# Kernel tuning notes

Measured on AMD Instinct MI355X. Metric: run time of the kernel, lower is better.

The kernel has to match this reference:

```python
import jax, jax.numpy as jnp
from jax import lax
import numpy as np

T = 16  # decode_times
NEG_SLOPE = 0.01  # LeakyReLU default


def setup_inputs() -> dict:
    key = jax.random.key(0)
    ks = jax.random.split(key, 8)
    H = 256  # hidden_size
    C = 256  # input_size
    O = 2    # linear_output_size
    s = 1.0 / np.sqrt(H)
    return {
        "x": jax.random.normal(ks[0], (8, C, 40, 40), jnp.float32),
        "hx": jnp.zeros((12800, H), jnp.float32),
        "cx": jnp.zeros((12800, H), jnp.float32),
        "W_ih": jax.random.uniform(ks[1], (4 * H, C), jnp.float32, -s, s),
        "W_hh": jax.random.uniform(ks[2], (4 * H, H), jnp.float32, -s, s),
        "b_ih": jax.random.uniform(ks[3], (4 * H,), jnp.float32, -s, s),
        "b_hh": jax.random.uniform(ks[4], (4 * H,), jnp.float32, -s, s),
        "W_lin": jax.random.uniform(ks[5], (O, H), jnp.float32, -s, s),
        "b_lin": jax.random.uniform(ks[6], (O,), jnp.float32, -s, s),
    }


def reference(x, hx, cx, W_ih, W_hh, b_ih, b_hh, W_lin, b_lin):
    bs, c, h, w = x.shape
    # BSxCxHxW -> (BS*H*W, C): same flattening as permute(0,2,3,1).reshape(-1, C)
    xf = jnp.transpose(x, (0, 2, 3, 1)).reshape(-1, c)
    # Input projection is identical every step (same x fed each time)
    x_proj = xf @ W_ih.T + b_ih + b_hh  # [N, 4H]

    def step(carry, _):
        hx, cx = carry
        gates = x_proj + hx @ W_hh.T  # [N, 4H]
        i, f, g, o = jnp.split(gates, 4, axis=-1)  # torch LSTMCell gate order
        i = jax.nn.sigmoid(i)
        f = jax.nn.sigmoid(f)
        g = jnp.tanh(g)
        o = jax.nn.sigmoid(o)
        cx = f * cx + i * g
        hx = o * jnp.tanh(cx)
        return (hx, cx), hx

    _, outs = lax.scan(step, (hx, cx), None, length=T)  # [T, N, H]
    # Dropout(0.1) is identity in eval mode; LeakyReLU then Linear head
    y = jax.nn.leaky_relu(outs, NEG_SLOPE)
    y = jnp.einsum('tnh,oh->tno', y, W_lin) + b_lin  # [T, N, O]
    y = y.reshape(T, bs, h, w, -1)
    return jnp.transpose(y, (1, 2, 3, 0, 4))  # [BS, H, W, T, O]
```

## Files before the change

### kernel.cpp

```cpp
#include <hip/hip_runtime.h>
#include <stdint.h>
#include <stddef.h>

typedef _Float16 half_t;
typedef half_t half8  __attribute__((ext_vector_type(8)));
typedef half_t half4v __attribute__((ext_vector_type(4)));
typedef float  f32x4  __attribute__((ext_vector_type(4)));

__device__ __forceinline__ float fast_sigmoid(float x) {
    float e = __builtin_amdgcn_exp2f(-1.44269504f * x);
    return __builtin_amdgcn_rcpf(1.0f + e);
}
__device__ __forceinline__ float fast_tanh(float x) {
    float e = __builtin_amdgcn_exp2f(2.88539008f * x);
    return 1.0f - 2.0f * __builtin_amdgcn_rcpf(1.0f + e);
}

__global__ __launch_bounds__(64) void shuffle_w_kernel(
    const float* __restrict__ W, half_t* __restrict__ out)
{
    const int blk = blockIdx.x;
    const int T = blk >> 3, kt = blk & 7;
    const int l = threadIdx.x;
    const int j = T * 16 + (l & 15);
    const int k0 = kt * 32 + ((l >> 4) << 3);
    half8 v;
#pragma unroll
    for (int e = 0; e < 8; ++e) v[e] = (half_t)W[j * 256 + k0 + e];
    *reinterpret_cast<half8*>(out + (size_t)(blk * 64 + l) * 8) = v;
}

__device__ __forceinline__ void gemm_pass(
    f32x4* acc, const half_t* __restrict__ lhx,
    const half_t* Ws, int Ta, int Tb, int Tc, int Td,
    int lm, int lg, int l)
{
    asm volatile("" : "+v"(Ws));
    const half_t* bp[4] = {
        Ws + (size_t)((Ta * 8) * 64 + l) * 8,
        Ws + (size_t)((Tb * 8) * 64 + l) * 8,
        Ws + (size_t)((Tc * 8) * 64 + l) * 8,
        Ws + (size_t)((Td * 8) * 64 + l) * 8 };
    half8 bA[4], bB[4];
#pragma unroll
    for (int n = 0; n < 4; ++n) bA[n] = *reinterpret_cast<const half8*>(bp[n]);

#pragma unroll 1
    for (int kt2 = 0; kt2 < 4; ++kt2) {
        const int kt = kt2 * 2;
#pragma unroll
        for (int n = 0; n < 4; ++n)
            bB[n] = *reinterpret_cast<const half8*>(bp[n] + (kt + 1) * 512);
        {
            half8 a[4];
#pragma unroll
            for (int mt = 0; mt < 4; ++mt) {
                const int p = mt * 16 + lm;
                const int k = (kt * 32 + lg * 8) ^ ((p & 7) << 4);
                a[mt] = *reinterpret_cast<const half8*>(&lhx[p * 256 + k]);
            }
#pragma unroll
            for (int n = 0; n < 4; ++n)
#pragma unroll
                for (int mt = 0; mt < 4; ++mt)
                    acc[mt * 4 + n] = __builtin_amdgcn_mfma_f32_16x16x32_f16(
                        a[mt], bA[n], acc[mt * 4 + n], 0, 0, 0);
        }
        __builtin_amdgcn_sched_barrier(0);
#pragma unroll
        for (int n = 0; n < 4; ++n)
            bA[n] = *reinterpret_cast<const half8*>(bp[n] + ((kt + 2) & 7) * 512);
        {
            half8 a[4];
#pragma unroll
            for (int mt = 0; mt < 4; ++mt) {
                const int p = mt * 16 + lm;
                const int k = ((kt + 1) * 32 + lg * 8) ^ ((p & 7) << 4);
                a[mt] = *reinterpret_cast<const half8*>(&lhx[p * 256 + k]);
            }
#pragma unroll
            for (int n = 0; n < 4; ++n)
#pragma unroll
                for (int mt = 0; mt < 4; ++mt)
                    acc[mt * 4 + n] = __builtin_amdgcn_mfma_f32_16x16x32_f16(
                        a[mt], bB[n], acc[mt * 4 + n], 0, 0, 0);
        }
        __builtin_amdgcn_sched_barrier(0);
    }
}

__global__ __launch_bounds__(512)
void lstm_kernel(
    const float* __restrict__ x,
    const float* __restrict__ hx0,
    const float* __restrict__ cx0,
    const float* __restrict__ b_ih,
    const float* __restrict__ b_hh,
    const float* __restrict__ W_lin,
    const float* __restrict__ b_lin,
    const half_t* __restrict__ Wih_s,
    const half_t* __restrict__ Whh_s,
    float* __restrict__ out)
{
    __shared__ __align__(16) half_t lds_hx[64 * 256];
    __shared__ __align__(16) half_t lds_xp[8 * 32 * 64 * 4];

    const int tid = threadIdx.x;
    const int w  = tid >> 6;
    const int l  = tid & 63;
    const int lm = l & 15;
    const int lg = l >> 4;
    const int w2 = w * 2;

    const int row0 = blockIdx.x * 64;
    const int bb_  = row0 / 1600;
    const int p0   = row0 % 1600;

    {
        const float* xin = x + (size_t)bb_ * 409600 + p0;
        for (int it = 0; it < 32; ++it) {
            int idx = it * 512 + tid;
            int p = idx & 63, c = idx >> 6;
            lds_hx[p * 256 + (c ^ ((p & 7) << 4))] = (half_t)xin[c * 1600 + p];
        }
    }
    __syncthreads();

    f32x4 acc[16];

#pragma unroll 1
    for (int pass = 0; pass < 2; ++pass) {
        const int gA = pass ? 0 : 16;
        const int gB = pass ? 32 : 48;
        const int Ta = gA + w2, Tb = Ta + 1;
        const int Tc = gB + w2, Td = Tc + 1;
        const int Tt[4] = {Ta, Tb, Tc, Td};
#pragma unroll
        for (int n = 0; n < 4; ++n) {
            int col = Tt[n] * 16 + lm;
            float bias = b_ih[col] + b_hh[col];
#pragma unroll
            for (int mt = 0; mt < 4; ++mt)
                acc[mt * 4 + n] = (f32x4){bias, bias, bias, bias};
        }
        gemm_pass(acc, lds_hx, Wih_s, Ta, Tb, Tc, Td, lm, lg, l);
#pragma unroll
        for (int f = 0; f < 16; ++f) {
            half4v xv;
#pragma unroll
            for (int r = 0; r < 4; ++r) xv[r] = (half_t)acc[f][r];
            *reinterpret_cast<half4v*>(
                &lds_xp[((w * 32 + pass * 16 + f) * 64 + l) * 4]) = xv;
        }
    }
    __syncthreads();

    {
        const float* hin = hx0 + (size_t)row0 * 256;
        for (int it = 0; it < 32; ++it) {
            int idx = it * 512 + tid;
            int c = idx & 255, p = idx >> 8;
            lds_hx[p * 256 + (c ^ ((p & 7) << 4))] = (half_t)hin[p * 256 + c];
        }
    }
    float cxr[32];
#pragma unroll
    for (int mt = 0; mt < 4; ++mt)
#pragma unroll
        for (int j = 0; j < 2; ++j)
#pragma unroll
            for (int r = 0; r < 4; ++r) {
                int p = mt * 16 + lg * 4 + r;
                int c = w * 32 + j * 16 + lm;
                cxr[(mt * 2 + j) * 4 + r] = cx0[(size_t)(row0 + p) * 256 + c];
            }
    const float blin0 = b_lin[0], blin1 = b_lin[1];
    __syncthreads();

#pragma unroll 1
    for (int t = 0; t < 16; ++t) {
        half4v og[8];

#pragma unroll
        for (int fc = 0; fc < 16; fc += 4) {
#pragma unroll
            for (int f = fc; f < fc + 4; ++f) {
                half4v u = *reinterpret_cast<const half4v*>(
                    &lds_xp[((w * 32 + f) * 64 + l) * 4]);
#pragma unroll
                for (int r = 0; r < 4; ++r) acc[f][r] = (float)u[r];
            }
            __builtin_amdgcn_sched_barrier(0);
        }
        gemm_pass(acc, lds_hx, Whh_s, 16 + w2, 17 + w2, 48 + w2, 49 + w2,
                  lm, lg, l);
#pragma unroll
        for (int mt = 0; mt < 4; ++mt)
#pragma unroll
            for (int j = 0; j < 2; ++j)
#pragma unroll
                for (int r = 0; r < 4; ++r) {
                    float fv = acc[mt * 4 + 0 + j][r];
                    float ov = acc[mt * 4 + 2 + j][r];
                    cxr[(mt * 2 + j) * 4 + r] *= fast_sigmoid(fv);
                    og[mt * 2 + j][r] = (half_t)ov;
                }
        __builtin_amdgcn_sched_barrier(0);

#pragma unroll
        for (int fc = 0; fc < 16; fc += 4) {
#pragma unroll
            for (int f = fc; f < fc + 4; ++f) {
                half4v u = *reinterpret_cast<const half4v*>(
                    &lds_xp[((w * 32 + 16 + f) * 64 + l) * 4]);
#pragma unroll
                for (int r = 0; r < 4; ++r) acc[f][r] = (float)u[r];
            }
            __builtin_amdgcn_sched_barrier(0);
        }
        gemm_pass(acc, lds_hx, Whh_s, w2, w2 + 1, 32 + w2, 33 + w2,
                  lm, lg, l);

        __syncthreads();

#pragma unroll
        for (int mt = 0; mt < 4; ++mt)
#pragma unroll
            for (int j = 0; j < 2; ++j)
#pragma unroll
                for (int r = 0; r < 4; ++r) {
                    const int ci = (mt * 2 + j) * 4 + r;
                    float iv = acc[mt * 4 + 0 + j][r];
                    float gv = acc[mt * 4 + 2 + j][r];
                    float cxn = cxr[ci] + fast_sigmoid(iv) * fast_tanh(gv);
                    cxr[ci] = cxn;
                    float so = fast_sigmoid((float)og[mt * 2 + j][r]);
                    float h = so * fast_tanh(cxn);
                    int p  = mt * 16 + lg * 4 + r;
                    int cc = w * 32 + j * 16 + lm;
                    lds_hx[p * 256 + (cc ^ ((p & 7) << 4))] = (half_t)h;
                }
        __syncthreads();

        {
            const int p = tid >> 3;
            const int o = (tid >> 2) & 1;
            const int q = tid & 3;
            const float* wl = W_lin + o * 256 + q * 64;
            asm volatile("" : "+v"(wl));
            float s = 0.0f;
#pragma unroll 2
            for (int cb = 0; cb < 16; ++cb) {
                int c0 = q * 64 + cb * 4;
                half4v u = *reinterpret_cast<const half4v*>(
                    &lds_hx[p * 256 + (c0 ^ ((p & 7) << 4))]);
                float4 wv = *reinterpret_cast<const float4*>(wl + cb * 4);
                float h0 = (float)u[0], h1 = (float)u[1];
                float h2 = (float)u[2], h3 = (float)u[3];
                s += fmaxf(h0, 0.01f * h0) * wv.x;
                s += fmaxf(h1, 0.01f * h1) * wv.y;
                s += fmaxf(h2, 0.01f * h2) * wv.z;
                s += fmaxf(h3, 0.01f * h3) * wv.w;
            }
            s += __shfl_xor(s, 1);
            s += __shfl_xor(s, 2);
            if (q == 0)
                out[((size_t)(row0 + p) * 16 + t) * 2 + o] =
                    s + (o ? blin1 : blin0);
        }
    }
}

extern "C" void kernel_launch(void* const* d_in, const int* in_sizes, int n_in,
                              void* d_out, int out_size, void* d_ws, size_t ws_size,
                              hipStream_t stream)
{
    const float* x    = (const float*)d_in[0];
    const float* hx   = (const float*)d_in[1];
    const float* cx   = (const float*)d_in[2];
    const float* Wih  = (const float*)d_in[3];
    const float* Whh  = (const float*)d_in[4];
    const float* bih  = (const float*)d_in[5];
    const float* bhh  = (const float*)d_in[6];
    const float* Wlin = (const float*)d_in[7];
    const float* blin = (const float*)d_in[8];
    float* out = (float*)d_out;

    half_t* wih_s = (half_t*)d_ws;
    half_t* whh_s = wih_s + 1024 * 256;

    shuffle_w_kernel<<<512, 64, 0, stream>>>(Wih, wih_s);
    shuffle_w_kernel<<<512, 64, 0, stream>>>(Whh, whh_s);
    lstm_kernel<<<200, 512, 0, stream>>>(x, hx, cx, bih, bhh, Wlin, blin,
                                         wih_s, whh_s, out);
}
```

Measured before the change: 253.6 us.

## Interleave output head and gate epilogue with recurrent GEMM MFMA passes

The gemm_pass loop is fully unrolled and takes a per-k-step callback, so non-MFMA work can be interleaved with the matrix instructions. The linear head for step t-1 now runs inside the first recurrent GEMM of step t, and the forget/output gate sigmoids run inside the second GEMM using a separate accumulator set. A final head pass handles the last timestep after the loop. This aims to hide VALU and LDS work behind MFMA latency and drops one barrier-separated phase per step, at the cost of a second accumulator array and higher register pressure, which could spill or lower occupancy.

```diff
diff --git a/kernel.cpp b/kernel.cpp
--- a/kernel.cpp
+++ b/kernel.cpp
@@ -30,10 +30,11 @@
     *reinterpret_cast<half8*>(out + (size_t)(blk * 64 + l) * 8) = v;
 }
 
+template <typename CoWork>
 __device__ __forceinline__ void gemm_pass(
     f32x4* acc, const half_t* __restrict__ lhx,
     const half_t* Ws, int Ta, int Tb, int Tc, int Td,
-    int lm, int lg, int l)
+    int lm, int lg, int l, CoWork&& cowork)
 {
     asm volatile("" : "+v"(Ws));
     const half_t* bp[4] = {
@@ -41,49 +42,34 @@
         Ws + (size_t)((Tb * 8) * 64 + l) * 8,
         Ws + (size_t)((Tc * 8) * 64 + l) * 8,
         Ws + (size_t)((Td * 8) * 64 + l) * 8 };
-    half8 bA[4], bB[4];
-#pragma unroll
-    for (int n = 0; n < 4; ++n) bA[n] = *reinterpret_cast<const half8*>(bp[n]);
-
-#pragma unroll 1
-    for (int kt2 = 0; kt2 < 4; ++kt2) {
-        const int kt = kt2 * 2;
+    half8 bC[4], bN[4];
+#pragma unroll
+    for (int n = 0; n < 4; ++n) bC[n] = *reinterpret_cast<const half8*>(bp[n]);
+
+#pragma unroll
+    for (int kt = 0; kt < 8; ++kt) {
+        if (kt < 7) {
+#pragma unroll
+            for (int n = 0; n < 4; ++n)
+                bN[n] = *reinterpret_cast<const half8*>(bp[n] + (kt + 1) * 512);
+        }
+        half8 a[4];
+#pragma unroll
+        for (int mt = 0; mt < 4; ++mt) {
+            const int p = mt * 16 + lm;
+            const int k = (kt * 32 + lg * 8) ^ ((p & 7) << 4);
+            a[mt] = *reinterpret_cast<const half8*>(&lhx[p * 256 + k]);
+        }
 #pragma unroll
         for (int n = 0; n < 4; ++n)
-            bB[n] = *reinterpret_cast<const half8*>(bp[n] + (kt + 1) * 512);
-        {
-            half8 a[4];
-#pragma unroll
-            for (int mt = 0; mt < 4; ++mt) {
-                const int p = mt * 16 + lm;
-                const int k = (kt * 32 + lg * 8) ^ ((p & 7) << 4);
-                a[mt] = *reinterpret_cast<const half8*>(&lhx[p * 256 + k]);
-            }
-#pragma unroll
-            for (int n = 0; n < 4; ++n)
-#pragma unroll
-                for (int mt = 0; mt < 4; ++mt)
-                    acc[mt * 4 + n] = __builtin_amdgcn_mfma_f32_16x16x32_f16(
-                        a[mt], bA[n], acc[mt * 4 + n], 0, 0, 0);
-        }
-        __builtin_amdgcn_sched_barrier(0);
-#pragma unroll
-        for (int n = 0; n < 4; ++n)
-            bA[n] = *reinterpret_cast<const half8*>(bp[n] + ((kt + 2) & 7) * 512);
-        {
-            half8 a[4];
-#pragma unroll
-            for (int mt = 0; mt < 4; ++mt) {
-                const int p = mt * 16 + lm;
-                const int k = ((kt + 1) * 32 + lg * 8) ^ ((p & 7) << 4);
-                a[mt] = *reinterpret_cast<const half8*>(&lhx[p * 256 + k]);
-            }
-#pragma unroll
-            for (int n = 0; n < 4; ++n)
-#pragma unroll
-                for (int mt = 0; mt < 4; ++mt)
-                    acc[mt * 4 + n] = __builtin_amdgcn_mfma_f32_16x16x32_f16(
-                        a[mt], bB[n], acc[mt * 4 + n], 0, 0, 0);
+#pragma unroll
+            for (int mt = 0; mt < 4; ++mt)
+                acc[mt * 4 + n] = __builtin_amdgcn_mfma_f32_16x16x32_f16(
+                    a[mt], bC[n], acc[mt * 4 + n], 0, 0, 0);
+        cowork(kt);
+        if (kt < 7) {
+#pragma unroll
+            for (int n = 0; n < 4; ++n) bC[n] = bN[n];
         }
         __builtin_amdgcn_sched_barrier(0);
     }
@@ -126,7 +112,8 @@
     }
     __syncthreads();
 
-    f32x4 acc[16];
+    f32x4 accA[16], accB[16];
+    auto nocw = [](int) {};
 
 #pragma unroll 1
     for (int pass = 0; pass < 2; ++pass) {
@@ -141,14 +128,14 @@
             float bias = b_ih[col] + b_hh[col];
 #pragma unroll
             for (int mt = 0; mt < 4; ++mt)
-                acc[mt * 4 + n] = (f32x4){bias, bias, bias, bias};
-        }
-        gemm_pass(acc, lds_hx, Wih_s, Ta, Tb, Tc, Td, lm, lg, l);
+                accA[mt * 4 + n] = (f32x4){bias, bias, bias, bias};
+        }
+        gemm_pass(accA, lds_hx, Wih_s, Ta, Tb, Tc, Td, lm, lg, l, nocw);
 #pragma unroll
         for (int f = 0; f < 16; ++f) {
             half4v xv;
 #pragma unroll
-            for (int r = 0; r < 4; ++r) xv[r] = (half_t)acc[f][r];
+            for (int r = 0; r < 4; ++r) xv[r] = (half_t)accA[f][r];
             *reinterpret_cast<half4v*>(
                 &lds_xp[((w * 32 + pass * 16 + f) * 64 + l) * 4]) = xv;
         }
@@ -175,12 +162,47 @@
                 cxr[(mt * 2 + j) * 4 + r] = cx0[(size_t)(row0 + p) * 256 + c];
             }
     const float blin0 = b_lin[0], blin1 = b_lin[1];
+    const int ph = tid >> 3;
+    const int ho = (tid >> 2) & 1;
+    const int hq = tid & 3;
     __syncthreads();
 
 #pragma unroll 1
     for (int t = 0; t < 16; ++t) {
         half4v og[8];
 
+        const float* wl = W_lin + ho * 256 + hq * 64;
+        asm volatile("" : "+v"(wl));
+        float hs = 0.0f;
+        float4 hwv0, hwv1;
+        if (t > 0) {
+            hwv0 = *reinterpret_cast<const float4*>(wl + 0);
+            hwv1 = *reinterpret_cast<const float4*>(wl + 4);
+        }
+        auto head_cw = [&](int wi) {
+            if (t > 0) {
+#pragma unroll
+                for (int ii = 0; ii < 2; ++ii) {
+                    int cb = wi * 2 + ii;
+                    int c0 = hq * 64 + cb * 4;
+                    half4v u = *reinterpret_cast<const half4v*>(
+                        &lds_hx[ph * 256 + (c0 ^ ((ph & 7) << 4))]);
+                    float4 wv = ii ? hwv1 : hwv0;
+                    if (cb + 2 < 16) {
+                        float4 nx = *reinterpret_cast<const float4*>(
+                            wl + (cb + 2) * 4);
+                        if (ii) hwv1 = nx; else hwv0 = nx;
+                    }
+                    float h0 = (float)u[0], h1 = (float)u[1];
+                    float h2 = (float)u[2], h3 = (float)u[3];
+                    hs += fmaxf(h0, 0.01f * h0) * wv.x;
+                    hs += fmaxf(h1, 0.01f * h1) * wv.y;
+                    hs += fmaxf(h2, 0.01f * h2) * wv.z;
+                    hs += fmaxf(h3, 0.01f * h3) * wv.w;
+                }
+            }
+        };
+
 #pragma unroll
         for (int fc = 0; fc < 16; fc += 4) {
 #pragma unroll
@@ -188,24 +210,31 @@
                 half4v u = *reinterpret_cast<const half4v*>(
                     &lds_xp[((w * 32 + f) * 64 + l) * 4]);
 #pragma unroll
-                for (int r = 0; r < 4; ++r) acc[f][r] = (float)u[r];
+                for (int r = 0; r < 4; ++r) accA[f][r] = (float)u[r];
             }
             __builtin_amdgcn_sched_barrier(0);
         }
-        gemm_pass(acc, lds_hx, Whh_s, 16 + w2, 17 + w2, 48 + w2, 49 + w2,
-                  lm, lg, l);
-#pragma unroll
-        for (int mt = 0; mt < 4; ++mt)
-#pragma unroll
-            for (int j = 0; j < 2; ++j)
-#pragma unroll
-                for (int r = 0; r < 4; ++r) {
-                    float fv = acc[mt * 4 + 0 + j][r];
-                    float ov = acc[mt * 4 + 2 + j][r];
-                    cxr[(mt * 2 + j) * 4 + r] *= fast_sigmoid(fv);
-                    og[mt * 2 + j][r] = (half_t)ov;
-                }
-        __builtin_amdgcn_sched_barrier(0);
+        gemm_pass(accA, lds_hx, Whh_s, 16 + w2, 17 + w2, 48 + w2, 49 + w2,
+                  lm, lg, l, head_cw);
+        if (t > 0) {
+            hs += __shfl_xor(hs, 1);
+            hs += __shfl_xor(hs, 2);
+            if (hq == 0)
+                out[((size_t)(row0 + ph) * 16 + (t - 1)) * 2 + ho] =
+                    hs + (ho ? blin1 : blin0);
+        }
+
+        auto epiA_cw = [&](int wi) {
+#pragma unroll
+            for (int k = 0; k < 4; ++k) {
+                int v = wi * 4 + k;
+                int mt = v >> 3, j = (v >> 2) & 1, r = v & 3;
+                float fv = accA[mt * 4 + 0 + j][r];
+                float ov = accA[mt * 4 + 2 + j][r];
+                cxr[(mt * 2 + j) * 4 + r] *= fast_sigmoid(fv);
+                og[mt * 2 + j][r] = (half_t)fast_sigmoid(ov);
+            }
+        };
 
 #pragma unroll
         for (int fc = 0; fc < 16; fc += 4) {
@@ -214,12 +243,12 @@
                 half4v u = *reinterpret_cast<const half4v*>(
                     &lds_xp[((w * 32 + 16 + f) * 64 + l) * 4]);
 #pragma unroll
-                for (int r = 0; r < 4; ++r) acc[f][r] = (float)u[r];
+                for (int r = 0; r < 4; ++r) accB[f][r] = (float)u[r];
             }
             __builtin_amdgcn_sched_barrier(0);
         }
-        gemm_pass(acc, lds_hx, Whh_s, w2, w2 + 1, 32 + w2, 33 + w2,
-                  lm, lg, l);
+        gemm_pass(accB, lds_hx, Whh_s, w2, w2 + 1, 32 + w2, 33 + w2,
+                  lm, lg, l, epiA_cw);
 
         __syncthreads();
 
@@ -230,44 +259,40 @@
 #pragma unroll
                 for (int r = 0; r < 4; ++r) {
                     const int ci = (mt * 2 + j) * 4 + r;
-                    float iv = acc[mt * 4 + 0 + j][r];
-                    float gv = acc[mt * 4 + 2 + j][r];
+                    float iv = accB[mt * 4 + 0 + j][r];
+                    float gv = accB[mt * 4 + 2 + j][r];
                     float cxn = cxr[ci] + fast_sigmoid(iv) * fast_tanh(gv);
                     cxr[ci] = cxn;
-                    float so = fast_sigmoid((float)og[mt * 2 + j][r]);
-                    float h = so * fast_tanh(cxn);
+                    float h = (float)og[mt * 2 + j][r] * fast_tanh(cxn);
                     int p  = mt * 16 + lg * 4 + r;
                     int cc = w * 32 + j * 16 + lm;
                     lds_hx[p * 256 + (cc ^ ((p & 7) << 4))] = (half_t)h;
                 }
         __syncthreads();
-
-        {
-            const int p = tid >> 3;
-            const int o = (tid >> 2) & 1;
-            const int q = tid & 3;
-            const float* wl = W_lin + o * 256 + q * 64;
-            asm volatile("" : "+v"(wl));
-            float s = 0.0f;
+    }
+
+    {
+        const float* wl = W_lin + ho * 256 + hq * 64;
+        asm volatile("" : "+v"(wl));
+        float s = 0.0f;
 #pragma unroll 2
-            for (int cb = 0; cb < 16; ++cb) {
-                int c0 = q * 64 + cb * 4;
-                half4v u = *reinterpret_cast<const half4v*>(
-                    &lds_hx[p * 256 + (c0 ^ ((p & 7) << 4))]);
-                float4 wv = *reinterpret_cast<const float4*>(wl + cb * 4);
-                float h0 = (float)u[0], h1 = (float)u[1];
-                float h2 = (float)u[2], h3 = (float)u[3];
-                s += fmaxf(h0, 0.01f * h0) * wv.x;
-                s += fmaxf(h1, 0.01f * h1) * wv.y;
-                s += fmaxf(h2, 0.01f * h2) * wv.z;
-                s += fmaxf(h3, 0.01f * h3) * wv.w;
-            }
-            s += __shfl_xor(s, 1);
-            s += __shfl_xor(s, 2);
-            if (q == 0)
-                out[((size_t)(row0 + p) * 16 + t) * 2 + o] =
-                    s + (o ? blin1 : blin0);
-        }
+        for (int cb = 0; cb < 16; ++cb) {
+            int c0 = hq * 64 + cb * 4;
+            half4v u = *reinterpret_cast<const half4v*>(
+                &lds_hx[ph * 256 + (c0 ^ ((ph & 7) << 4))]);
+            float4 wv = *reinterpret_cast<const float4*>(wl + cb * 4);
+            float h0 = (float)u[0], h1 = (float)u[1];
+            float h2 = (float)u[2], h3 = (float)u[3];
+            s += fmaxf(h0, 0.01f * h0) * wv.x;
+            s += fmaxf(h1, 0.01f * h1) * wv.y;
+            s += fmaxf(h2, 0.01f * h2) * wv.z;
+            s += fmaxf(h3, 0.01f * h3) * wv.w;
+        }
+        s += __shfl_xor(s, 1);
+        s += __shfl_xor(s, 2);
+        if (hq == 0)
+            out[((size_t)(row0 + ph) * 16 + 15) * 2 + ho] =
+                s + (ho ? blin1 : blin0);
     }
 }
 
```

Measured after the change: 318.2 us. 25.5% more time.

## Overlap linear head of previous step with first recurrent GEMM pass

Applied to the files above, without the earlier changes.

The LeakyReLU+Linear head for step t-1 now runs interleaved with the MFMA loop of the first W_hh GEMM pass at step t, through a per-k-tile callback. It no longer runs as a separate phase after the hidden-state update barrier, and the last step's head runs after the loop. The aim is to hide the head's LDS reads, W_lin loads and FMAs under matrix-core work and remove one serialized phase per step. The cost is higher register pressure from the prefetched weights and accumulator inside the GEMM loop, which could reduce scheduling quality.

```diff
diff --git a/kernel.cpp b/kernel.cpp
--- a/kernel.cpp
+++ b/kernel.cpp
@@ -30,10 +30,11 @@
     *reinterpret_cast<half8*>(out + (size_t)(blk * 64 + l) * 8) = v;
 }
 
+template <typename CoWork>
 __device__ __forceinline__ void gemm_pass(
     f32x4* acc, const half_t* __restrict__ lhx,
     const half_t* Ws, int Ta, int Tb, int Tc, int Td,
-    int lm, int lg, int l)
+    int lm, int lg, int l, CoWork&& cowork)
 {
     asm volatile("" : "+v"(Ws));
     const half_t* bp[4] = {
@@ -66,6 +67,7 @@
                     acc[mt * 4 + n] = __builtin_amdgcn_mfma_f32_16x16x32_f16(
                         a[mt], bA[n], acc[mt * 4 + n], 0, 0, 0);
         }
+        cowork(kt);
         __builtin_amdgcn_sched_barrier(0);
 #pragma unroll
         for (int n = 0; n < 4; ++n)
@@ -85,6 +87,7 @@
                     acc[mt * 4 + n] = __builtin_amdgcn_mfma_f32_16x16x32_f16(
                         a[mt], bB[n], acc[mt * 4 + n], 0, 0, 0);
         }
+        cowork(kt + 1);
         __builtin_amdgcn_sched_barrier(0);
     }
 }
@@ -127,6 +130,7 @@
     __syncthreads();
 
     f32x4 acc[16];
+    auto nocw = [](int) {};
 
 #pragma unroll 1
     for (int pass = 0; pass < 2; ++pass) {
@@ -143,7 +147,7 @@
             for (int mt = 0; mt < 4; ++mt)
                 acc[mt * 4 + n] = (f32x4){bias, bias, bias, bias};
         }
-        gemm_pass(acc, lds_hx, Wih_s, Ta, Tb, Tc, Td, lm, lg, l);
+        gemm_pass(acc, lds_hx, Wih_s, Ta, Tb, Tc, Td, lm, lg, l, nocw);
 #pragma unroll
         for (int f = 0; f < 16; ++f) {
             half4v xv;
@@ -175,12 +179,47 @@
                 cxr[(mt * 2 + j) * 4 + r] = cx0[(size_t)(row0 + p) * 256 + c];
             }
     const float blin0 = b_lin[0], blin1 = b_lin[1];
+    const int ph = tid >> 3;
+    const int ho = (tid >> 2) & 1;
+    const int hq = tid & 3;
     __syncthreads();
 
 #pragma unroll 1
     for (int t = 0; t < 16; ++t) {
         half4v og[8];
 
+        const float* wl = W_lin + ho * 256 + hq * 64;
+        asm volatile("" : "+v"(wl));
+        float hs = 0.0f;
+        float4 hwv0, hwv1;
+        if (t > 0) {
+            hwv0 = *reinterpret_cast<const float4*>(wl + 0);
+            hwv1 = *reinterpret_cast<const float4*>(wl + 4);
+        }
+        auto head_cw = [&](int wi) {
+            if (t > 0) {
+#pragma unroll
+                for (int ii = 0; ii < 2; ++ii) {
+                    int cb = wi * 2 + ii;
+                    int c0 = hq * 64 + cb * 4;
+                    half4v u = *reinterpret_cast<const half4v*>(
+                        &lds_hx[ph * 256 + (c0 ^ ((ph & 7) << 4))]);
+                    float4 wv = ii ? hwv1 : hwv0;
+                    if (cb + 2 < 16) {
+                        float4 nx = *reinterpret_cast<const float4*>(
+                            wl + (cb + 2) * 4);
+                        if (ii) hwv1 = nx; else hwv0 = nx;
+                    }
+                    float h0 = (float)u[0], h1 = (float)u[1];
+                    float h2 = (float)u[2], h3 = (float)u[3];
+                    hs += fmaxf(h0, 0.01f * h0) * wv.x;
+                    hs += fmaxf(h1, 0.01f * h1) * wv.y;
+                    hs += fmaxf(h2, 0.01f * h2) * wv.z;
+                    hs += fmaxf(h3, 0.01f * h3) * wv.w;
+                }
+            }
+        };
+
 #pragma unroll
         for (int fc = 0; fc < 16; fc += 4) {
 #pragma unroll
@@ -193,7 +232,15 @@
             __builtin_amdgcn_sched_barrier(0);
         }
         gemm_pass(acc, lds_hx, Whh_s, 16 + w2, 17 + w2, 48 + w2, 49 + w2,
-                  lm, lg, l);
+                  lm, lg, l, head_cw);
+        if (t > 0) {
+            hs += __shfl_xor(hs, 1);
+            hs += __shfl_xor(hs, 2);
+            if (hq == 0)
+                out[((size_t)(row0 + ph) * 16 + (t - 1)) * 2 + ho] =
+                    hs + (ho ? blin1 : blin0);
+        }
+
 #pragma unroll
         for (int mt = 0; mt < 4; ++mt)
 #pragma unroll
@@ -219,7 +266,7 @@
             __builtin_amdgcn_sched_barrier(0);
         }
         gemm_pass(acc, lds_hx, Whh_s, w2, w2 + 1, 32 + w2, 33 + w2,
-                  lm, lg, l);
+                  lm, lg, l, nocw);
 
         __syncthreads();
 
@@ -241,33 +288,30 @@
                     lds_hx[p * 256 + (cc ^ ((p & 7) << 4))] = (half_t)h;
                 }
         __syncthreads();
-
-        {
-            const int p = tid >> 3;
-            const int o = (tid >> 2) & 1;
-            const int q = tid & 3;
-            const float* wl = W_lin + o * 256 + q * 64;
-            asm volatile("" : "+v"(wl));
-            float s = 0.0f;
+    }
+
+    {
+        const float* wl = W_lin + ho * 256 + hq * 64;
+        asm volatile("" : "+v"(wl));
+        float s = 0.0f;
 #pragma unroll 2
-            for (int cb = 0; cb < 16; ++cb) {
-                int c0 = q * 64 + cb * 4;
-                half4v u = *reinterpret_cast<const half4v*>(
-                    &lds_hx[p * 256 + (c0 ^ ((p & 7) << 4))]);
-                float4 wv = *reinterpret_cast<const float4*>(wl + cb * 4);
-                float h0 = (float)u[0], h1 = (float)u[1];
-                float h2 = (float)u[2], h3 = (float)u[3];
-                s += fmaxf(h0, 0.01f * h0) * wv.x;
-                s += fmaxf(h1, 0.01f * h1) * wv.y;
-                s += fmaxf(h2, 0.01f * h2) * wv.z;
-                s += fmaxf(h3, 0.01f * h3) * wv.w;
-            }
-            s += __shfl_xor(s, 1);
-            s += __shfl_xor(s, 2);
-            if (q == 0)
-                out[((size_t)(row0 + p) * 16 + t) * 2 + o] =
-                    s + (o ? blin1 : blin0);
-        }
+        for (int cb = 0; cb < 16; ++cb) {
+            int c0 = hq * 64 + cb * 4;
+            half4v u = *reinterpret_cast<const half4v*>(
+                &lds_hx[ph * 256 + (c0 ^ ((ph & 7) << 4))]);
+            float4 wv = *reinterpret_cast<const float4*>(wl + cb * 4);
+            float h0 = (float)u[0], h1 = (float)u[1];
+            float h2 = (float)u[2], h3 = (float)u[3];
+            s += fmaxf(h0, 0.01f * h0) * wv.x;
+            s += fmaxf(h1, 0.01f * h1) * wv.y;
+            s += fmaxf(h2, 0.01f * h2) * wv.z;
+            s += fmaxf(h3, 0.01f * h3) * wv.w;
+        }
+        s += __shfl_xor(s, 1);
+        s += __shfl_xor(s, 2);
+        if (hq == 0)
+            out[((size_t)(row0 + ph) * 16 + 15) * 2 + ho] =
+                s + (ho ? blin1 : blin0);
     }
 }
 
```

After: 245.1 us. 3.3% less time.
